# Optimization experiments

Measured on AMD Instinct MI355X. Metric: run time of the kernel, lower is better.

The kernel has to match this reference:

```python
import jax, jax.numpy as jnp
import numpy as np

H, D, HID = 8, 16, 128
B, L = 2, 512
SCALE = D ** -0.5
EPS = 1e-5


def _ln(x, g, b):
    mu = jnp.mean(x, axis=-1, keepdims=True)
    var = jnp.mean((x - mu) ** 2, axis=-1, keepdims=True)
    return (x - mu) * jax.lax.rsqrt(var + EPS) * g + b


def setup_inputs() -> dict:
    key = jax.random.key(0)
    ks = jax.random.split(key, 24)
    HD = H * D
    s = 0.02
    inp = {
        'x': jax.random.normal(ks[0], (B, L, HID), jnp.float32),
        'r': jax.random.normal(ks[1], (B, L, L, HID), jnp.float32),
        'mask': jnp.ones((B, L, L), jnp.bool_),
        'ln1_g': jnp.ones((HID,), jnp.float32),
        'ln1_b': jnp.zeros((HID,), jnp.float32),
        'Wq': jax.random.normal(ks[2], (HID, HD), jnp.float32) * s,
        'bq': jnp.zeros((HD,), jnp.float32),
        'Wk': jax.random.normal(ks[3], (HID, HD), jnp.float32) * s,
        'Wv': jax.random.normal(ks[4], (HID, HD), jnp.float32) * s,
        'bv': jnp.zeros((HD,), jnp.float32),
        'Wkr': jax.random.normal(ks[5], (HID, HD), jnp.float32) * s,
        'Wvr': jax.random.normal(ks[6], (HID, HD), jnp.float32) * s,
        'bvr': jnp.zeros((HD,), jnp.float32),
        'Ws': jax.random.normal(ks[7], (HID, HD), jnp.float32) * s,
        'bs': jnp.zeros((HD,), jnp.float32),
        'Wg': jax.random.normal(ks[8], (HD + HID, HD), jnp.float32) * s,
        'bg': jnp.zeros((HD,), jnp.float32),
        'Wo': jax.random.normal(ks[9], (HD, HID), jnp.float32) * s,
        'bo': jnp.zeros((HID,), jnp.float32),
        'ln2_g': jnp.ones((HID,), jnp.float32),
        'ln2_b': jnp.zeros((HID,), jnp.float32),
        'W1': jax.random.normal(ks[10], (HID, 4 * HID), jnp.float32) * s,
        'b1': jnp.zeros((4 * HID,), jnp.float32),
        'W2': jax.random.normal(ks[11], (4 * HID, HID), jnp.float32) * s,
        'b2': jnp.zeros((HID,), jnp.float32),
    }
    return inp


def reference(x, r, mask, ln1_g, ln1_b, Wq, bq, Wk, Wv, bv, Wkr, Wvr, bvr,
              Ws, bs, Wg, bg, Wo, bo, ln2_g, ln2_b, W1, b1, W2, b2):
    b_, l_ = x.shape[0], x.shape[1]
    h = _ln(x, ln1_g, ln1_b)  # x_src = x_dst = LN(x)
    # projections (q broadcast over lenk, k/v broadcast over lenq)
    q = (h @ Wq + bq).reshape(b_, l_, 1, H, D)
    k = (h @ Wk).reshape(b_, 1, l_, H, D)
    v = (h @ Wv + bv).reshape(b_, 1, l_, H, D)
    rk = (r @ Wkr).reshape(b_, l_, l_, H, D)
    rv = (r @ Wvr + bvr).reshape(b_, l_, l_, H, D)
    k = k + rk
    v = v + rv
    sim = jnp.sum(q * k, axis=-1) * SCALE  # [B, lenq, lenk, H]
    sim = jnp.where(mask[..., None], sim, jnp.float32(-100.0))
    attn = jax.nn.softmax(sim, axis=-2)  # over lenk
    out = jnp.sum(v * attn[..., None], axis=-3)  # [B, lenq, H, D]
    inputs = out.reshape(b_, l_, H * D)
    cat = jnp.concatenate([inputs, h], axis=-1)
    g = jax.nn.sigmoid(cat @ Wg + bg)
    agg = inputs + g * ((h @ Ws + bs) - inputs)
    x1 = x + agg @ Wo + bo
    x2 = _ln(x1, ln2_g, ln2_b)
    ff = jax.nn.relu(x2 @ W1 + b1) @ W2 + b2
    return x1 + ff
```

## Files before the change

kernel.cpp:

```cpp
#include <hip/hip_runtime.h>

#define L_    512
#define B_    2
#define HID_  128
#define NROW_ 131072
#define EPS_  1e-5f
#define SCLE2_ 0.3606737602222409f

typedef __attribute__((ext_vector_type(8))) short          short8v;
typedef __attribute__((ext_vector_type(8))) unsigned short ushort8v;
typedef __attribute__((ext_vector_type(4))) unsigned short ushort4v;
typedef __attribute__((ext_vector_type(4))) float          f32x4;

static __device__ __forceinline__ unsigned short f2bf(float f) {
    unsigned int u = __float_as_uint(f);
    u = u + 0x7FFFu + ((u >> 16) & 1u);
    return (unsigned short)(u >> 16);
}
static __device__ __forceinline__ float bf2f(unsigned short u) {
    return __uint_as_float(((unsigned int)u) << 16);
}

__global__ void wprep_kernel(const float* __restrict__ Wvr, unsigned short* __restrict__ wvT)
{
    int o = blockIdx.x;
    int c = threadIdx.x;
    wvT[o * 128 + c] = f2bf(Wvr[c * 128 + o]);
}

__global__ __launch_bounds__(128)
void pre_kernel(const float* __restrict__ x,
                const float* __restrict__ g1, const float* __restrict__ b1ln,
                const float* __restrict__ Wq, const float* __restrict__ bq,
                const float* __restrict__ Wk,
                const float* __restrict__ Wv, const float* __restrict__ bv,
                const float* __restrict__ Ws, const float* __restrict__ bs,
                const float* __restrict__ Wkr, const float* __restrict__ bvr,
                float* __restrict__ h_out, float* __restrict__ q_out,
                float* __restrict__ k_out, float* __restrict__ vbT,
                float* __restrict__ s_out, unsigned short* __restrict__ wkqT)
{
    __shared__ float sh[128];
    __shared__ float red[2];
    const int row = blockIdx.x;
    const int o = threadIdx.x;
    float xo = x[row * 128 + o];
    float s = xo;
    #pragma unroll
    for (int m = 32; m; m >>= 1) s += __shfl_xor(s, m);
    if ((o & 63) == 0) red[o >> 6] = s;
    __syncthreads();
    float mu = (red[0] + red[1]) * 0.0078125f;
    float dx = xo - mu;
    float v2 = dx * dx;
    #pragma unroll
    for (int m = 32; m; m >>= 1) v2 += __shfl_xor(v2, m);
    __syncthreads();
    if ((o & 63) == 0) red[o >> 6] = v2;
    __syncthreads();
    float var = (red[0] + red[1]) * 0.0078125f;
    float ho = dx * rsqrtf(var + EPS_) * g1[o] + b1ln[o];
    sh[o] = ho;
    h_out[row * 128 + o] = ho;
    __syncthreads();
    float aq = bq[o], ak = 0.f, av = bv[o] + bvr[o], as2 = bs[o];
    for (int c = 0; c < 128; ++c) {
        float hc = sh[c];
        aq  = fmaf(hc, Wq[c * 128 + o], aq);
        ak  = fmaf(hc, Wk[c * 128 + o], ak);
        av  = fmaf(hc, Wv[c * 128 + o], av);
        as2 = fmaf(hc, Ws[c * 128 + o], as2);
    }
    q_out[row * 128 + o] = aq;
    k_out[row * 128 + o] = ak;
    vbT[((size_t)(row >> 9) * 128 + o) * 512 + (row & 511)] = av;
    s_out[row * 128 + o] = as2;
    __syncthreads();
    sh[o] = aq;
    __syncthreads();
    const float* wrow = Wkr + o * 128;
    #pragma unroll
    for (int hh = 0; hh < 8; ++hh) {
        float s2 = 0.f;
        #pragma unroll
        for (int d = 0; d < 16; ++d) s2 = fmaf(wrow[hh * 16 + d], sh[hh * 16 + d], s2);
        wkqT[(size_t)row * 1024 + hh * 128 + o] = f2bf(s2 * SCLE2_);
    }
}

__global__ __launch_bounds__(512)
void simb_kernel(const float* __restrict__ q, const float* __restrict__ kb,
                 unsigned short* __restrict__ simb)
{
    __shared__ float qs[4][128];
    const int b  = blockIdx.x >> 7;
    const int i0 = (blockIdx.x & 127) * 4;
    const int j  = threadIdx.x;
    qs[j >> 7][j & 127] = q[((size_t)(b * L_ + i0)) * 128 + j];
    __syncthreads();
    const float* krow = kb + ((size_t)(b * L_ + j)) * 128;
    float dots[4][8];
    #pragma unroll
    for (int i = 0; i < 4; ++i)
        #pragma unroll
        for (int h = 0; h < 8; ++h) dots[i][h] = 0.f;
    #pragma unroll
    for (int c4 = 0; c4 < 32; ++c4) {
        float4 kv = *(const float4*)(krow + c4 * 4);
        int h = c4 >> 2;
        #pragma unroll
        for (int i = 0; i < 4; ++i) {
            const float* qp = &qs[i][c4 * 4];
            dots[i][h] = fmaf(qp[0], kv.x, fmaf(qp[1], kv.y,
                         fmaf(qp[2], kv.z, fmaf(qp[3], kv.w, dots[i][h]))));
        }
    }
    #pragma unroll
    for (int i = 0; i < 4; ++i)
        #pragma unroll
        for (int h = 0; h < 8; ++h)
            simb[(((size_t)(b * L_ + i0 + i)) * 8 + h) * 512 + j] = f2bf(dots[i][h] * SCLE2_);
}

__global__ __launch_bounds__(512, 6)
void attn_kernel(const float* __restrict__ r,
                 const float* __restrict__ vbT,
                 const unsigned short* __restrict__ wvT,
                 const unsigned short* __restrict__ wkqT,
                 const unsigned short* __restrict__ simb,
                 float* __restrict__ opart,
                 float* __restrict__ lpart)
{
    __shared__ __align__(16) unsigned short sR[2][64 * 128];

    const int tid  = threadIdx.x;
    const int lane = tid & 63;
    const int w    = tid >> 6;
    const int g    = lane >> 4;
    const int cl   = lane & 15;
    const int bid  = blockIdx.x;
    const int jq   = bid >> 10;
    const int bi   = bid & 1023;
    const int b    = bi >> 9;
    const int jbase = jq * 128;

    const float* rflat = r + (size_t)bi * (L_ * HID_) + (size_t)jbase * HID_;

    float4 rrA[4], rrB[4];
    #pragma unroll
    for (int k2 = 0; k2 < 4; ++k2) rrA[k2] = *(const float4*)(rflat + k2 * 2048 + tid * 4);
    #pragma unroll
    for (int k2 = 0; k2 < 4; ++k2) rrB[k2] = *(const float4*)(rflat + 8192 + k2 * 2048 + tid * 4);

    short8v wvB[4], wkqB[4];
    {
        const unsigned short* p = wvT + (w * 16 + cl) * 128 + g * 8;
        #pragma unroll
        for (int ks = 0; ks < 4; ++ks) wvB[ks] = *(const short8v*)(p + ks * 32);
    }
    {
        const unsigned short* p = wkqT + (size_t)bi * 1024 + w * 128 + g * 8;
        #pragma unroll
        for (int ks = 0; ks < 4; ++ks) wkqB[ks] = *(const short8v*)(p + ks * 32);
    }

    {
        char* rb0 = (char*)sR[0];
        char* rb1 = (char*)sR[1];
        #pragma unroll
        for (int k2 = 0; k2 < 4; ++k2) {
            int f  = k2 * 2048 + tid * 4;
            int rw = f >> 7;
            int st = ((rw << 8) + ((f & 127) << 1)) ^ ((rw & 7) << 4);
            ushort4v a4 = { f2bf(rrA[k2].x), f2bf(rrA[k2].y), f2bf(rrA[k2].z), f2bf(rrA[k2].w) };
            ushort4v b4 = { f2bf(rrB[k2].x), f2bf(rrB[k2].y), f2bf(rrB[k2].z), f2bf(rrB[k2].w) };
            *(ushort4v*)(rb0 + st) = a4;
            *(ushort4v*)(rb1 + st) = b4;
        }
    }
    __syncthreads();

    const unsigned short* simbB = simb + ((size_t)bi * 8 + w) * 512 + jbase;
    const float*          vbTb  = vbT + ((size_t)b * 128 + w * 16 + cl) * 512 + jbase;
    float outp = 0.f, lsum = 0.f;

    #pragma unroll
    for (int t = 0; t < 2; ++t) {
        const char* sRc = (const char*)sR[t];
        const unsigned short* sb = simbB + t * 64;
        const float*          vp = vbTb  + t * 64;
        #pragma unroll
        for (int jb = 0; jb < 4; ++jb) {
            ushort4v s4 = *(const ushort4v*)(sb + jb * 16 + g * 4);
            float4   vv = *(const float4*)(vp + jb * 16 + g * 4);
            const int ar  = jb * 16 + cl;
            const int ab  = ar << 8;
            const int asw = (ar & 7) << 4;
            f32x4 accS = {0.f, 0.f, 0.f, 0.f};
            f32x4 accV = { vv.x, vv.y, vv.z, vv.w };
            #pragma unroll
            for (int ks = 0; ks < 4; ++ks) {
                short8v af = *(const short8v*)(sRc + ((ab + ks * 64 + g * 16) ^ asw));
                accS = __builtin_amdgcn_mfma_f32_16x16x32_bf16(af, wkqB[ks], accS, 0, 0, 0);
                accV = __builtin_amdgcn_mfma_f32_16x16x32_bf16(af, wvB[ks],  accV, 0, 0, 0);
            }
            #pragma unroll
            for (int rg = 0; rg < 4; ++rg) {
                float p = __builtin_amdgcn_exp2f(accS[rg] + bf2f(s4[rg]));
                lsum += p;
                outp  = fmaf(p, accV[rg], outp);
            }
        }
    }

    outp += __shfl_xor(outp, 16); outp += __shfl_xor(outp, 32);
    lsum += __shfl_xor(lsum, 16); lsum += __shfl_xor(lsum, 32);
    if (lane < 16) opart[(size_t)jq * NROW_ + (size_t)bi * 128 + w * 16 + cl] = outp;
    if (lane == 0) lpart[jq * (B_ * L_ * 8) + bi * 8 + w] = lsum;
}

__global__ __launch_bounds__(512)
void post_kernel(const float* __restrict__ x, const float* __restrict__ h,
                 const float* __restrict__ opart, const float* __restrict__ lpart,
                 const float* __restrict__ hs,
                 const float* __restrict__ Wg, const float* __restrict__ bg,
                 const float* __restrict__ Wo, const float* __restrict__ bo,
                 const float* __restrict__ g2, const float* __restrict__ b2g,
                 const float* __restrict__ W1, const float* __restrict__ b1f,
                 const float* __restrict__ W2, const float* __restrict__ b2f,
                 float* __restrict__ out)
{
    __shared__ float cat[4][256];
    __shared__ float agg[4][128];
    __shared__ float x2s[4][128];
    __shared__ float hid[4][512];
    __shared__ float red[4][2];
    const int ri  = threadIdx.x >> 7;
    const int o   = threadIdx.x & 127;
    const int wv2 = (threadIdx.x >> 6) & 1;
    const int row = blockIdx.x * 4 + ri;
    float osum = 0.f, lsum = 0.f;
    #pragma unroll
    for (int jqq = 0; jqq < 4; ++jqq) {
        osum += opart[(size_t)jqq * NROW_ + (size_t)row * 128 + o];
        lsum += lpart[jqq * (B_ * L_ * 8) + row * 8 + (o >> 4)];
    }
    float atto = osum / lsum;
    cat[ri][o] = atto;
    cat[ri][128 + o] = h[(size_t)row * 128 + o];
    __syncthreads();
    float a0 = 0.f, a1 = 0.f, a2 = 0.f, a3 = 0.f;
    for (int c = 0; c < 256; c += 4) {
        a0 = fmaf(cat[ri][c],     Wg[(c)     * 128 + o], a0);
        a1 = fmaf(cat[ri][c + 1], Wg[(c + 1) * 128 + o], a1);
        a2 = fmaf(cat[ri][c + 2], Wg[(c + 2) * 128 + o], a2);
        a3 = fmaf(cat[ri][c + 3], Wg[(c + 3) * 128 + o], a3);
    }
    float ag = bg[o] + ((a0 + a1) + (a2 + a3));
    float gg = 1.f / (1.f + __expf(-ag));
    agg[ri][o] = atto + gg * (hs[(size_t)row * 128 + o] - atto);
    __syncthreads();
    float b0 = 0.f, b1v = 0.f, b2v = 0.f, b3 = 0.f;
    for (int c = 0; c < 128; c += 4) {
        b0  = fmaf(agg[ri][c],     Wo[(c)     * 128 + o], b0);
        b1v = fmaf(agg[ri][c + 1], Wo[(c + 1) * 128 + o], b1v);
        b2v = fmaf(agg[ri][c + 2], Wo[(c + 2) * 128 + o], b2v);
        b3  = fmaf(agg[ri][c + 3], Wo[(c + 3) * 128 + o], b3);
    }
    float x1 = x[(size_t)row * 128 + o] + bo[o] + ((b0 + b1v) + (b2v + b3));
    float s = x1;
    #pragma unroll
    for (int m = 32; m; m >>= 1) s += __shfl_xor(s, m);
    if ((threadIdx.x & 63) == 0) red[ri][wv2] = s;
    __syncthreads();
    float mu = (red[ri][0] + red[ri][1]) * 0.0078125f;
    float dx = x1 - mu;
    float v2 = dx * dx;
    #pragma unroll
    for (int m = 32; m; m >>= 1) v2 += __shfl_xor(v2, m);
    __syncthreads();
    if ((threadIdx.x & 63) == 0) red[ri][wv2] = v2;
    __syncthreads();
    float var = (red[ri][0] + red[ri][1]) * 0.0078125f;
    float x2v = dx * rsqrtf(var + EPS_) * g2[o] + b2g[o];
    x2s[ri][o] = x2v;
    __syncthreads();
    {
        float h0 = b1f[o], h1 = b1f[128 + o], h2 = b1f[256 + o], h3 = b1f[384 + o];
        for (int c = 0; c < 128; ++c) {
            float xc = x2s[ri][c];
            h0 = fmaf(xc, W1[c * 512 + o],       h0);
            h1 = fmaf(xc, W1[c * 512 + 128 + o], h1);
            h2 = fmaf(xc, W1[c * 512 + 256 + o], h2);
            h3 = fmaf(xc, W1[c * 512 + 384 + o], h3);
        }
        hid[ri][o]       = fmaxf(h0, 0.f);
        hid[ri][128 + o] = fmaxf(h1, 0.f);
        hid[ri][256 + o] = fmaxf(h2, 0.f);
        hid[ri][384 + o] = fmaxf(h3, 0.f);
    }
    __syncthreads();
    float c0 = 0.f, c1 = 0.f, c2 = 0.f, c3 = 0.f;
    for (int u = 0; u < 512; u += 4) {
        c0 = fmaf(hid[ri][u],     W2[(u)     * 128 + o], c0);
        c1 = fmaf(hid[ri][u + 1], W2[(u + 1) * 128 + o], c1);
        c2 = fmaf(hid[ri][u + 2], W2[(u + 2) * 128 + o], c2);
        c3 = fmaf(hid[ri][u + 3], W2[(u + 3) * 128 + o], c3);
    }
    out[(size_t)row * 128 + o] = x1 + b2f[o] + ((c0 + c1) + (c2 + c3));
}

extern "C" void kernel_launch(void* const* d_in, const int* in_sizes, int n_in,
                              void* d_out, int out_size, void* d_ws, size_t ws_size,
                              hipStream_t stream)
{
    (void)in_sizes; (void)n_in; (void)out_size; (void)ws_size;
    const float* x    = (const float*)d_in[0];
    const float* r    = (const float*)d_in[1];
    const float* ln1g = (const float*)d_in[3];
    const float* ln1b = (const float*)d_in[4];
    const float* Wq   = (const float*)d_in[5];
    const float* bq   = (const float*)d_in[6];
    const float* Wk   = (const float*)d_in[7];
    const float* Wv   = (const float*)d_in[8];
    const float* bv   = (const float*)d_in[9];
    const float* Wkr  = (const float*)d_in[10];
    const float* Wvr  = (const float*)d_in[11];
    const float* bvr  = (const float*)d_in[12];
    const float* Ws   = (const float*)d_in[13];
    const float* bs   = (const float*)d_in[14];
    const float* Wg   = (const float*)d_in[15];
    const float* bg   = (const float*)d_in[16];
    const float* Wo   = (const float*)d_in[17];
    const float* bo   = (const float*)d_in[18];
    const float* g2   = (const float*)d_in[19];
    const float* b2g  = (const float*)d_in[20];
    const float* W1   = (const float*)d_in[21];
    const float* b1   = (const float*)d_in[22];
    const float* W2   = (const float*)d_in[23];
    const float* b2   = (const float*)d_in[24];

    float* ws = (float*)d_ws;
    float* hbuf  = ws;
    float* qbuf  = hbuf + NROW_;
    float* kbuf  = qbuf + NROW_;
    float* vbT   = kbuf + NROW_;
    float* sbuf  = vbT + NROW_;
    float* opart = sbuf + NROW_;
    float* lpart = opart + 4 * NROW_;
    unsigned short* wkqT = (unsigned short*)(lpart + 4 * B_ * L_ * 8);
    unsigned short* simb = wkqT + (size_t)B_ * L_ * 1024;
    unsigned short* wvT  = simb + (size_t)B_ * L_ * 8 * 512;

    hipLaunchKernelGGL(wprep_kernel, dim3(128), dim3(128), 0, stream, Wvr, wvT);
    hipLaunchKernelGGL(pre_kernel, dim3(B_ * L_), dim3(128), 0, stream,
                       x, ln1g, ln1b, Wq, bq, Wk, Wv, bv, Ws, bs, Wkr, bvr,
                       hbuf, qbuf, kbuf, vbT, sbuf, wkqT);
    hipLaunchKernelGGL(simb_kernel, dim3(B_ * 128), dim3(512), 0, stream,
                       qbuf, kbuf, simb);
    hipLaunchKernelGGL(attn_kernel, dim3(4 * B_ * L_), dim3(512), 0, stream,
                       r, vbT, wvT, wkqT, simb, opart, lpart);
    hipLaunchKernelGGL(post_kernel, dim3(B_ * L_ / 4), dim3(512), 0, stream,
                       x, hbuf, opart, lpart, sbuf, Wg, bg, Wo, bo, g2, b2g, W1, b1, W2, b2,
                       (float*)d_out);
}
```

Before: 158.8 us.

## Fold weight prep into pre kernel and overlap second r tile store with compute

Removes the separate wvT transpose launch by having the first 128 blocks of pre_kernel write the bf16-transposed Wvr. In attn_kernel the first r half is now stored to LDS and computed before the second half is converted and stored, so the conversion overlaps with MFMA work. The LDS fragment loads are hoisted ahead of the MFMA chain, and MFMA issue priority is raised with s_setprio. The occupancy hint drops from 6 to 4 waves, which gives more registers per thread but allows fewer resident blocks to hide memory latency.

```diff
diff --git a/kernel.cpp b/kernel.cpp
--- a/kernel.cpp
+++ b/kernel.cpp
@@ -19,13 +19,6 @@
 }
 static __device__ __forceinline__ float bf2f(unsigned short u) {
     return __uint_as_float(((unsigned int)u) << 16);
-}
-
-__global__ void wprep_kernel(const float* __restrict__ Wvr, unsigned short* __restrict__ wvT)
-{
-    int o = blockIdx.x;
-    int c = threadIdx.x;
-    wvT[o * 128 + c] = f2bf(Wvr[c * 128 + o]);
 }
 
 __global__ __launch_bounds__(128)
@@ -36,14 +29,17 @@
                 const float* __restrict__ Wv, const float* __restrict__ bv,
                 const float* __restrict__ Ws, const float* __restrict__ bs,
                 const float* __restrict__ Wkr, const float* __restrict__ bvr,
+                const float* __restrict__ Wvr,
                 float* __restrict__ h_out, float* __restrict__ q_out,
                 float* __restrict__ k_out, float* __restrict__ vbT,
-                float* __restrict__ s_out, unsigned short* __restrict__ wkqT)
+                float* __restrict__ s_out, unsigned short* __restrict__ wkqT,
+                unsigned short* __restrict__ wvT)
 {
     __shared__ float sh[128];
     __shared__ float red[2];
     const int row = blockIdx.x;
     const int o = threadIdx.x;
+    if (row < 128) wvT[row * 128 + o] = f2bf(Wvr[o * 128 + row]);
     float xo = x[row * 128 + o];
     float s = xo;
     #pragma unroll
@@ -122,7 +118,7 @@
             simb[(((size_t)(b * L_ + i0 + i)) * 8 + h) * 512 + j] = f2bf(dots[i][h] * SCLE2_);
 }
 
-__global__ __launch_bounds__(512, 6)
+__global__ __launch_bounds__(512, 4)
 void attn_kernel(const float* __restrict__ r,
                  const float* __restrict__ vbT,
                  const unsigned short* __restrict__ wvT,
@@ -144,14 +140,6 @@
     const int b    = bi >> 9;
     const int jbase = jq * 128;
 
-    const float* rflat = r + (size_t)bi * (L_ * HID_) + (size_t)jbase * HID_;
-
-    float4 rrA[4], rrB[4];
-    #pragma unroll
-    for (int k2 = 0; k2 < 4; ++k2) rrA[k2] = *(const float4*)(rflat + k2 * 2048 + tid * 4);
-    #pragma unroll
-    for (int k2 = 0; k2 < 4; ++k2) rrB[k2] = *(const float4*)(rflat + 8192 + k2 * 2048 + tid * 4);
-
     short8v wvB[4], wkqB[4];
     {
         const unsigned short* p = wvT + (w * 16 + cl) * 128 + g * 8;
@@ -164,46 +152,56 @@
         for (int ks = 0; ks < 4; ++ks) wkqB[ks] = *(const short8v*)(p + ks * 32);
     }
 
-    {
-        char* rb0 = (char*)sR[0];
-        char* rb1 = (char*)sR[1];
+    const float*          rflat = r    + (size_t)bi * (L_ * HID_) + (size_t)jbase * HID_;
+    const float*          vbTb  = vbT  + ((size_t)b * 128 + w * 16 + cl) * 512 + jbase;
+    const unsigned short* simbB = simb + ((size_t)bi * 8 + w) * 512 + jbase;
+
+    int stb[4];
+    #pragma unroll
+    for (int k2 = 0; k2 < 4; ++k2) {
+        int f = k2 * 2048 + tid * 4;
+        int rw = f >> 7;
+        stb[k2] = ((rw << 8) + ((f & 127) << 1)) ^ ((rw & 7) << 4);
+    }
+
+    float outp = 0.f, lsum = 0.f;
+
+    auto R_LOAD = [&](int t, float4* rr) {
+        const float* s = rflat + t * 8192;
+        #pragma unroll
+        for (int k2 = 0; k2 < 4; ++k2) rr[k2] = *(const float4*)(s + k2 * 2048 + tid * 4);
+    };
+    auto STORE = [&](int buf, const float4* rr) {
+        char* rb = (char*)sR[buf];
         #pragma unroll
         for (int k2 = 0; k2 < 4; ++k2) {
-            int f  = k2 * 2048 + tid * 4;
-            int rw = f >> 7;
-            int st = ((rw << 8) + ((f & 127) << 1)) ^ ((rw & 7) << 4);
-            ushort4v a4 = { f2bf(rrA[k2].x), f2bf(rrA[k2].y), f2bf(rrA[k2].z), f2bf(rrA[k2].w) };
-            ushort4v b4 = { f2bf(rrB[k2].x), f2bf(rrB[k2].y), f2bf(rrB[k2].z), f2bf(rrB[k2].w) };
-            *(ushort4v*)(rb0 + st) = a4;
-            *(ushort4v*)(rb1 + st) = b4;
+            ushort4v v4 = { f2bf(rr[k2].x), f2bf(rr[k2].y), f2bf(rr[k2].z), f2bf(rr[k2].w) };
+            *(ushort4v*)(rb + stb[k2]) = v4;
         }
-    }
-    __syncthreads();
-
-    const unsigned short* simbB = simb + ((size_t)bi * 8 + w) * 512 + jbase;
-    const float*          vbTb  = vbT + ((size_t)b * 128 + w * 16 + cl) * 512 + jbase;
-    float outp = 0.f, lsum = 0.f;
-
-    #pragma unroll
-    for (int t = 0; t < 2; ++t) {
-        const char* sRc = (const char*)sR[t];
-        const unsigned short* sb = simbB + t * 64;
-        const float*          vp = vbTb  + t * 64;
+    };
+
+    auto COMPUTE = [&](int buf, int j0) {
+        const char* sRc = (const char*)sR[buf];
         #pragma unroll
         for (int jb = 0; jb < 4; ++jb) {
-            ushort4v s4 = *(const ushort4v*)(sb + jb * 16 + g * 4);
-            float4   vv = *(const float4*)(vp + jb * 16 + g * 4);
+            ushort4v s4 = *(const ushort4v*)(simbB + j0 + jb * 16 + g * 4);
+            float4   vv = *(const float4*)(vbTb + j0 + jb * 16 + g * 4);
             const int ar  = jb * 16 + cl;
             const int ab  = ar << 8;
             const int asw = (ar & 7) << 4;
+            short8v af[4];
+            #pragma unroll
+            for (int ks = 0; ks < 4; ++ks)
+                af[ks] = *(const short8v*)(sRc + ((ab + ks * 64 + g * 16) ^ asw));
             f32x4 accS = {0.f, 0.f, 0.f, 0.f};
             f32x4 accV = { vv.x, vv.y, vv.z, vv.w };
+            __builtin_amdgcn_s_setprio(1);
             #pragma unroll
             for (int ks = 0; ks < 4; ++ks) {
-                short8v af = *(const short8v*)(sRc + ((ab + ks * 64 + g * 16) ^ asw));
-                accS = __builtin_amdgcn_mfma_f32_16x16x32_bf16(af, wkqB[ks], accS, 0, 0, 0);
-                accV = __builtin_amdgcn_mfma_f32_16x16x32_bf16(af, wvB[ks],  accV, 0, 0, 0);
+                accS = __builtin_amdgcn_mfma_f32_16x16x32_bf16(af[ks], wkqB[ks], accS, 0, 0, 0);
+                accV = __builtin_amdgcn_mfma_f32_16x16x32_bf16(af[ks], wvB[ks],  accV, 0, 0, 0);
             }
+            __builtin_amdgcn_s_setprio(0);
             #pragma unroll
             for (int rg = 0; rg < 4; ++rg) {
                 float p = __builtin_amdgcn_exp2f(accS[rg] + bf2f(s4[rg]));
@@ -211,7 +209,17 @@
                 outp  = fmaf(p, accV[rg], outp);
             }
         }
-    }
+    };
+
+    float4 rrA[4], rrB[4];
+    R_LOAD(0, rrA);
+    R_LOAD(1, rrB);
+    STORE(0, rrA);
+    __syncthreads();
+    COMPUTE(0, 0);
+    STORE(1, rrB);
+    __syncthreads();
+    COMPUTE(1, 64);
 
     outp += __shfl_xor(outp, 16); outp += __shfl_xor(outp, 32);
     lsum += __shfl_xor(lsum, 16); lsum += __shfl_xor(lsum, 32);
@@ -352,10 +360,9 @@
     unsigned short* simb = wkqT + (size_t)B_ * L_ * 1024;
     unsigned short* wvT  = simb + (size_t)B_ * L_ * 8 * 512;
 
-    hipLaunchKernelGGL(wprep_kernel, dim3(128), dim3(128), 0, stream, Wvr, wvT);
     hipLaunchKernelGGL(pre_kernel, dim3(B_ * L_), dim3(128), 0, stream,
-                       x, ln1g, ln1b, Wq, bq, Wk, Wv, bv, Ws, bs, Wkr, bvr,
-                       hbuf, qbuf, kbuf, vbT, sbuf, wkqT);
+                       x, ln1g, ln1b, Wq, bq, Wk, Wv, bv, Ws, bs, Wkr, bvr, Wvr,
+                       hbuf, qbuf, kbuf, vbT, sbuf, wkqT, wvT);
     hipLaunchKernelGGL(simb_kernel, dim3(B_ * 128), dim3(512), 0, stream,
                        qbuf, kbuf, simb);
     hipLaunchKernelGGL(attn_kernel, dim3(4 * B_ * L_), dim3(512), 0, stream,
```

New measurement: 143.1 us. -9.9%, faster.
